# Kernel tuning notes

Hardware: AMD Instinct MI355X
Metric: run time of the kernel (lower is better)

## Reference

```python
import jax, jax.numpy as jnp
import numpy as np

D_MODEL = 1024
D_STATE = 16
D_CONV = 4
EXPAND = 2
D_INNER = EXPAND * D_MODEL
BATCH = 2
SEQ = 4096


def setup_inputs() -> dict:
    key = jax.random.key(0)
    ks = jax.random.split(key, 8)
    def w(k, shape, fan_in):
        return jax.random.normal(k, shape, jnp.float32) * (fan_in ** -0.5)
    x = jax.random.normal(ks[0], (BATCH, SEQ, D_MODEL), jnp.float32)
    in_proj_w = w(ks[1], (2 * D_INNER, D_MODEL), D_MODEL)
    conv_w = w(ks[2], (D_INNER, 1, D_CONV), D_CONV)          # depthwise conv kernel (OIH, groups=D_INNER)
    conv_b = jnp.zeros((D_INNER,), jnp.float32)
    x_proj_w = w(ks[3], (1 + 2 * D_STATE, D_INNER), D_INNER)
    dt_proj_w = w(ks[4], (D_INNER, 1), D_STATE)               # Linear(1 -> d_inner), see notes
    dt_proj_b = jnp.zeros((D_INNER,), jnp.float32)
    A_log = jnp.log(jnp.tile(jnp.arange(1, D_STATE + 1, dtype=jnp.float32)[None, :], (D_INNER, 1)))
    D = jnp.ones((D_INNER,), jnp.float32)
    out_proj_w = w(ks[5], (D_MODEL, D_INNER), D_INNER)
    return dict(x=x, in_proj_w=in_proj_w, conv_w=conv_w, conv_b=conv_b,
                x_proj_w=x_proj_w, dt_proj_w=dt_proj_w, dt_proj_b=dt_proj_b,
                A_log=A_log, D=D, out_proj_w=out_proj_w)


def _selective_scan(xs, delta, Bm, Cm, A, D):
    # xs, delta: [B, L, d_inner]; Bm, Cm: [B, L, d_state]; A: [d_inner, d_state]
    def step(h, inp):
        x_t, d_t, b_t, c_t = inp                      # [B,di],[B,di],[B,n],[B,n]
        dA = jnp.exp(d_t[..., None] * A)              # [B, di, n]
        h = dA * h + (d_t * x_t)[..., None] * b_t[:, None, :]
        y = jnp.einsum('bdn,bn->bd', h, c_t) + D * x_t
        return h, y
    h0 = jnp.zeros((xs.shape[0], xs.shape[2], A.shape[1]), xs.dtype)
    seq = (jnp.swapaxes(xs, 0, 1), jnp.swapaxes(delta, 0, 1),
           jnp.swapaxes(Bm, 0, 1), jnp.swapaxes(Cm, 0, 1))
    _, ys = jax.lax.scan(step, h0, seq)               # ys: [L, B, di]
    return jnp.swapaxes(ys, 0, 1)


def _mamba(x, in_proj_w, conv_w, conv_b, x_proj_w, dt_proj_w, dt_proj_b, A_log, D, out_proj_w):
    xz = x @ in_proj_w.T                               # [B, L, 2*di]
    xc, z = jnp.split(xz, 2, axis=-1)
    # causal depthwise conv (pad left d_conv-1, truncate to seq_len)
    u = jnp.swapaxes(xc, 1, 2)                         # [B, di, L]
    u = jax.lax.conv_general_dilated(
        u, conv_w, window_strides=(1,), padding=[(D_CONV - 1, 0)],
        feature_group_count=D_INNER, dimension_numbers=('NCH', 'OIH', 'NCH'))
    u = u + conv_b[None, :, None]
    xs = jax.nn.silu(jnp.swapaxes(u, 1, 2))            # [B, L, di]
    dbc = xs @ x_proj_w.T                              # [B, L, 1+2n]
    delta_raw = dbc[..., :1]
    Bm = dbc[..., 1:1 + D_STATE]
    Cm = dbc[..., 1 + D_STATE:]
    delta = jax.nn.softplus(delta_raw @ dt_proj_w.T + dt_proj_b)   # [B, L, di]
    A = -jnp.exp(A_log)
    y = _selective_scan(xs, delta, Bm, Cm, A, D)
    return (y * jax.nn.silu(z)) @ out_proj_w.T


def reference(x, in_proj_w, conv_w, conv_b, x_proj_w, dt_proj_w, dt_proj_b, A_log, D, out_proj_w):
    return _mamba(x, in_proj_w, conv_w, conv_b, x_proj_w, dt_proj_w, dt_proj_b, A_log, D, out_proj_w)
```

## Files before the change

kernel.cpp:

```cpp
#include <hip/hip_runtime.h>
#include <hip/hip_bf16.h>
#include <stdint.h>

typedef __bf16 bf16x8 __attribute__((ext_vector_type(8)));
typedef float  f32x4  __attribute__((ext_vector_type(4)));
typedef float  f32x2  __attribute__((ext_vector_type(2)));
typedef unsigned short u16x8 __attribute__((ext_vector_type(8)));

#define TC 32
#define NC 128
#define TH 16

__device__ __forceinline__ unsigned short f2bf(float f) {
  unsigned u = __builtin_bit_cast(unsigned, f);
  unsigned r = (u + 0x7fffu + ((u >> 16) & 1u)) >> 16;
  return (unsigned short)r;
}
__device__ __forceinline__ float bf2f(unsigned short s) {
  unsigned u = ((unsigned)s) << 16;
  return __builtin_bit_cast(float, u);
}

__device__ __forceinline__ void gload_lds16(const void* g, void* l) {
  __builtin_amdgcn_global_load_lds(
      (const __attribute__((address_space(1))) unsigned int*)(g),
      (__attribute__((address_space(3))) unsigned int*)(l),
      16, 0, 0);
}

__global__ __launch_bounds__(256) void prep_k(
    const float4* __restrict__ x, const float4* __restrict__ ipw,
    const float4* __restrict__ opw, const float* __restrict__ xpw,
    ushort4* __restrict__ xb, ushort4* __restrict__ wb1,
    ushort4* __restrict__ wb2, unsigned short* __restrict__ xwp)
{
  const int r = blockIdx.y;
  int i = blockIdx.x * 256 + threadIdx.x;
  const int stride = gridDim.x * 256;
  if (r == 0) {
    for (; i < 2097152; i += stride) {
      float4 v = x[i]; ushort4 o;
      o.x = f2bf(v.x); o.y = f2bf(v.y); o.z = f2bf(v.z); o.w = f2bf(v.w);
      xb[i] = o;
    }
  } else if (r == 1) {
    for (; i < 1048576; i += stride) {
      float4 v = ipw[i]; ushort4 o;
      o.x = f2bf(v.x); o.y = f2bf(v.y); o.z = f2bf(v.z); o.w = f2bf(v.w);
      wb1[i] = o;
    }
  } else if (r == 2) {
    for (; i < 524288; i += stride) {
      float4 v = opw[i]; ushort4 o;
      o.x = f2bf(v.x); o.y = f2bf(v.y); o.z = f2bf(v.z); o.w = f2bf(v.w);
      wb2[i] = o;
    }
  } else {
    for (; i < 262144; i += stride) {
      int row = i >> 11, col = i & 2047;
      xwp[i] = (row < 33) ? f2bf(xpw[row * 2048 + col]) : (unsigned short)0;
    }
  }
}

template <bool BF16OUT, bool SWZ>
__global__ __launch_bounds__(512) void gemm8p(
    const unsigned short* __restrict__ A, const unsigned short* __restrict__ B,
    void* __restrict__ Cv, int M, int N, int K)
{
  __shared__ __align__(16) unsigned short As[2][2][8192];
  __shared__ __align__(16) unsigned short Bs[2][2][8192];
  const int tid = threadIdx.x;

  const int grid_m = M >> 8, grid_n = N >> 8;
  const int nwg = grid_m * grid_n;
  int wid = blockIdx.x;
  if (SWZ) { int q = nwg >> 3; wid = (wid & 7) * q + (wid >> 3); }
  const int GM = 8;
  const int nig = GM * grid_n;
  const int gidg = wid / nig;
  const int rem = wid - gidg * nig;
  const int fm = gidg * GM;
  const int gsz = (grid_m - fm < GM) ? (grid_m - fm) : GM;
  const int pm = fm + rem % gsz;
  const int pn = rem / gsz;
  const int m0 = pm << 8, n0 = pn << 8;

  const int NT = K >> 6;

  const int wq = tid >> 6, l = tid & 63;
  const int wr2 = wq >> 2, wc2 = wq & 3;
  const int lr = l & 15, q16 = l >> 4;
  const int sw = lr & 7;

  const unsigned short* aH0 = A + (size_t)m0 * K;
  const unsigned short* aH1 = A + (size_t)(m0 + 128) * K;
  const unsigned short* bH0 = B + (size_t)n0 * K;
  const unsigned short* bH1 = B + (size_t)(n0 + 128) * K;

#define STAGE8(srcbase, dstp, kt)                                              \
  { _Pragma("unroll") for (int i = 0; i < 2; ++i) {                            \
      int q = tid + 512 * i; int rw = q >> 3; int ssl = (q & 7) ^ (rw & 7);    \
      gload_lds16((srcbase) + (size_t)rw * K + (size_t)(kt) * 64 + ssl * 8,    \
                  (dstp) + q * 8); } }

#define LDA8(dd, MH)                                                           \
  { _Pragma("unroll") for (int mi = 0; mi < 4; ++mi) {                         \
      int ar = (wr2 * 64 + mi * 16 + lr) * 64;                                 \
      _Pragma("unroll") for (int ks = 0; ks < 2; ++ks)                         \
        af[mi][ks] = *(const bf16x8*)&As[dd][MH][ar + (((ks * 4 + q16) ^ sw) << 3)]; } }

#define LDB8(dd, NH)                                                           \
  { _Pragma("unroll") for (int ni = 0; ni < 2; ++ni) {                         \
      int br = (wc2 * 32 + ni * 16 + lr) * 64;                                 \
      _Pragma("unroll") for (int ks = 0; ks < 2; ++ks)                         \
        bf[NH][ni][ks] = *(const bf16x8*)&Bs[dd][NH][br + (((ks * 4 + q16) ^ sw) << 3)]; } }

#define MMA8(MH, NH)                                                           \
  { __builtin_amdgcn_s_setprio(1);                                             \
    _Pragma("unroll") for (int mi = 0; mi < 4; ++mi)                           \
    _Pragma("unroll") for (int ni = 0; ni < 2; ++ni)                           \
    _Pragma("unroll") for (int ks = 0; ks < 2; ++ks)                           \
      acc[MH][NH][mi][ni] = __builtin_amdgcn_mfma_f32_16x16x32_bf16(           \
          af[mi][ks], bf[NH][ni][ks], acc[MH][NH][mi][ni], 0, 0, 0);           \
    __builtin_amdgcn_s_setprio(0); }

  f32x4 acc[2][2][4][2];
#pragma unroll
  for (int a = 0; a < 2; ++a)
#pragma unroll
    for (int b = 0; b < 2; ++b)
#pragma unroll
      for (int c = 0; c < 4; ++c)
#pragma unroll
        for (int d = 0; d < 2; ++d)
          acc[a][b][c][d] = (f32x4){0.f, 0.f, 0.f, 0.f};

  bf16x8 af[4][2];
  bf16x8 bf[2][2][2];

  STAGE8(aH0, As[0][0], 0);
  STAGE8(bH1, Bs[0][1], 0);
  STAGE8(aH1, As[0][1], 0);
  STAGE8(bH0, Bs[0][0], 0);
  if (NT > 1) {
    STAGE8(aH0, As[1][0], 1);
    STAGE8(bH1, Bs[1][1], 1);
    asm volatile("s_waitcnt vmcnt(4)" ::: "memory");
  } else {
    asm volatile("s_waitcnt vmcnt(0)" ::: "memory");
  }
  __builtin_amdgcn_s_barrier();

  for (int t = 0; t < NT; ++t) {
    const int d = t & 1;
    LDA8(d, 0); LDB8(d, 0);
    if (t + 1 < NT) STAGE8(aH1, As[(t + 1) & 1][1], t + 1);
    MMA8(0, 0);
    __builtin_amdgcn_s_barrier();
    LDB8(d, 1);
    if (t + 1 < NT) STAGE8(bH0, Bs[(t + 1) & 1][0], t + 1);
    MMA8(0, 1);
    __builtin_amdgcn_s_barrier();
    LDA8(d, 1);
    if (t + 2 < NT) STAGE8(aH0, As[d][0], t + 2);
    MMA8(1, 1);
    __builtin_amdgcn_s_barrier();
    if (t + 2 < NT) STAGE8(bH1, Bs[d][1], t + 2);
    MMA8(1, 0);
    if (t + 2 < NT) asm volatile("s_waitcnt vmcnt(4)" ::: "memory");
    else            asm volatile("s_waitcnt vmcnt(0)" ::: "memory");
    __builtin_amdgcn_s_barrier();
  }

#pragma unroll
  for (int mh = 0; mh < 2; ++mh)
#pragma unroll
    for (int nh = 0; nh < 2; ++nh)
#pragma unroll
      for (int mi = 0; mi < 4; ++mi)
#pragma unroll
        for (int ni = 0; ni < 2; ++ni) {
          int gr = m0 + mh * 128 + wr2 * 64 + mi * 16 + q16 * 4;
          int gc = n0 + nh * 128 + wc2 * 32 + ni * 16 + lr;
#pragma unroll
          for (int j = 0; j < 4; ++j) {
            if (BF16OUT)
              ((unsigned short*)Cv)[(size_t)(gr + j) * N + gc] = f2bf(acc[mh][nh][mi][ni][j]);
            else
              ((float*)Cv)[(size_t)(gr + j) * N + gc] = acc[mh][nh][mi][ni][j];
          }
        }
#undef STAGE8
#undef LDA8
#undef LDB8
#undef MMA8
}

template <bool BF16OUT, bool SWZ>
__global__ __launch_bounds__(256) void gemm2p(
    const unsigned short* __restrict__ A, const unsigned short* __restrict__ B,
    void* __restrict__ Cv, int M, int N, int K)
{
  __shared__ __align__(16) unsigned short AsB[3 * 128 * 32];
  __shared__ __align__(16) unsigned short BsB[3 * 128 * 32];
  const int tid = threadIdx.x;

  const int grid_m = M >> 7, grid_n = N >> 7;
  const int nwg = grid_m * grid_n;
  int wid = blockIdx.x;
  if (SWZ) { int q = nwg >> 3; wid = (wid & 7) * q + (wid >> 3); }
  const int GM = 16;
  const int nig = GM * grid_n;
  const int gidg = wid / nig;
  const int rem = wid - gidg * nig;
  const int fm = gidg * GM;
  const int gsz = (grid_m - fm < GM) ? (grid_m - fm) : GM;
  const int pm = fm + rem % gsz;
  const int pn = rem / gsz;
  const int m0 = pm << 7, n0 = pn << 7;

  const int kseg = K / gridDim.z;
  const int kbeg = blockIdx.z * kseg;
  const int NT = kseg >> 5;

  const int w = tid >> 6, l = tid & 63;
  const int wr = w >> 1, wc = w & 1;
  const int lr = l & 15, kk = (l >> 4) * 8;

  f32x4 acc[4][4];
#pragma unroll
  for (int mi = 0; mi < 4; ++mi)
#pragma unroll
    for (int ni = 0; ni < 4; ++ni)
      acc[mi][ni] = (f32x4){0.f, 0.f, 0.f, 0.f};

#pragma unroll
  for (int tt = 0; tt < 2; ++tt) {
    unsigned short* as = AsB + tt * 4096;
    unsigned short* bs = BsB + tt * 4096;
    int k0 = kbeg + tt * 32;
#pragma unroll
    for (int i = 0; i < 2; ++i) {
      int q = tid + 256 * i;
      int row = q >> 2, sub = (q & 3) ^ ((q >> 3) & 3);
      gload_lds16(A + (size_t)(m0 + row) * K + k0 + sub * 8, as + q * 8);
      gload_lds16(B + (size_t)(n0 + row) * K + k0 + sub * 8, bs + q * 8);
    }
  }
  asm volatile("s_waitcnt vmcnt(4)\n\ts_barrier" ::: "memory");

  for (int t = 0; t < NT; ++t) {
    if (t + 2 < NT) {
      unsigned short* as = AsB + ((t + 2) % 3) * 4096;
      unsigned short* bs = BsB + ((t + 2) % 3) * 4096;
      int k0 = kbeg + (t + 2) * 32;
#pragma unroll
      for (int i = 0; i < 2; ++i) {
        int q = tid + 256 * i;
        int row = q >> 2, sub = (q & 3) ^ ((q >> 3) & 3);
        gload_lds16(A + (size_t)(m0 + row) * K + k0 + sub * 8, as + q * 8);
        gload_lds16(B + (size_t)(n0 + row) * K + k0 + sub * 8, bs + q * 8);
      }
    }
    const unsigned short* as = AsB + (t % 3) * 4096;
    const unsigned short* bs = BsB + (t % 3) * 4096;
    bf16x8 af[4], bfr[4];
#pragma unroll
    for (int mi = 0; mi < 4; ++mi) {
      int row = wr * 64 + mi * 16 + lr;
      int col = kk ^ (((row >> 1) & 3) << 3);
      af[mi] = *(const bf16x8*)&as[row * 32 + col];
    }
#pragma unroll
    for (int ni = 0; ni < 4; ++ni) {
      int row = wc * 64 + ni * 16 + lr;
      int col = kk ^ (((row >> 1) & 3) << 3);
      bfr[ni] = *(const bf16x8*)&bs[row * 32 + col];
    }
    __builtin_amdgcn_s_setprio(1);
#pragma unroll
    for (int mi = 0; mi < 4; ++mi)
#pragma unroll
      for (int ni = 0; ni < 4; ++ni)
        acc[mi][ni] = __builtin_amdgcn_mfma_f32_16x16x32_bf16(af[mi], bfr[ni], acc[mi][ni], 0, 0, 0);
    __builtin_amdgcn_s_setprio(0);
    if (t + 1 < NT) {
      if (t + 2 < NT) asm volatile("s_waitcnt vmcnt(4)\n\ts_barrier" ::: "memory");
      else            asm volatile("s_waitcnt vmcnt(0)\n\ts_barrier" ::: "memory");
    }
  }

#pragma unroll
  for (int mi = 0; mi < 4; ++mi)
#pragma unroll
    for (int ni = 0; ni < 4; ++ni) {
      int gr = m0 + wr * 64 + mi * 16 + (l >> 4) * 4;
      int gc = n0 + wc * 64 + ni * 16 + (l & 15);
#pragma unroll
      for (int j = 0; j < 4; ++j) {
        if (BF16OUT)
          ((unsigned short*)Cv)[(size_t)(gr + j) * N + gc] = f2bf(acc[mi][ni][j]);
        else
          ((float*)Cv + (size_t)blockIdx.z * M * N)[(size_t)(gr + j) * N + gc] = acc[mi][ni][j];
      }
    }
}

__global__ __launch_bounds__(256) void redux4_k(const float4* __restrict__ part,
                                                float4* __restrict__ out) {
  int i = blockIdx.x * 256 + threadIdx.x;
  const int STR = 262144;
  float4 a = part[i], b = part[i + STR], c = part[i + 2 * STR], d = part[i + 3 * STR];
  out[i] = make_float4(a.x + b.x + c.x + d.x, a.y + b.y + c.y + d.y,
                       a.z + b.z + c.z + d.z, a.w + b.w + c.w + d.w);
}

#define CONV_L 16
__global__ __launch_bounds__(256) void conv_silu_k(
    const unsigned short* __restrict__ xzb, const float* __restrict__ cw,
    const float* __restrict__ cb, unsigned short* __restrict__ xsb)
{
  const int b = blockIdx.y;
  const int l0 = blockIdx.x * CONV_L;
  const int d = threadIdx.x * 8;
  float w[4][8], bias[8];
#pragma unroll
  for (int i = 0; i < 8; ++i) {
    bias[i] = cb[d + i];
#pragma unroll
    for (int j = 0; j < 4; ++j) w[j][i] = cw[(d + i) * 4 + j];
  }
  const size_t rb = (size_t)b * 4096;
  float win[3][8];
#pragma unroll
  for (int j = 0; j < 3; ++j) {
    int l = l0 - 3 + j;
    if (l >= 0) {
      u16x8 v = *(const u16x8*)(xzb + (rb + l) * 4096 + d);
#pragma unroll
      for (int i = 0; i < 8; ++i) win[j][i] = bf2f(v[i]);
    } else {
#pragma unroll
      for (int i = 0; i < 8; ++i) win[j][i] = 0.f;
    }
  }
  for (int l = l0; l < l0 + CONV_L; ++l) {
    u16x8 v = *(const u16x8*)(xzb + (rb + l) * 4096 + d);
    float cur[8]; u16x8 ob;
#pragma unroll
    for (int i = 0; i < 8; ++i) {
      cur[i] = bf2f(v[i]);
      float u = bias[i] + w[0][i] * win[0][i] + w[1][i] * win[1][i]
                        + w[2][i] * win[2][i] + w[3][i] * cur[i];
      float s = u / (1.f + __expf(-u));
      ob[i] = f2bf(s);
    }
    *(u16x8*)(xsb + (rb + l) * 2048 + d) = ob;
#pragma unroll
    for (int i = 0; i < 8; ++i) { win[0][i] = win[1][i]; win[1][i] = win[2][i]; win[2][i] = cur[i]; }
  }
}

__global__ __launch_bounds__(256) void scan_p1(
    const unsigned short* __restrict__ xsb16, const float* __restrict__ dbc,
    const float* __restrict__ dtw, const float* __restrict__ dtb,
    const float* __restrict__ alog,
    float* __restrict__ Sg, float* __restrict__ cdg)
{
  const int chunk = blockIdx.x;
  const int d0 = blockIdx.y * 256;
  const int b = blockIdx.z;
  const int tid = threadIdx.x;
  const size_t rowbase = (size_t)b * 4096 + chunk * TC;

  __shared__ __align__(16) unsigned short xsS[TH][256];
  __shared__ __align__(16) float bS[TC][16];
  __shared__ float drS[TC];

  if (tid < TC) drS[tid] = dbc[(rowbase + tid) * 128];
  for (int i = tid; i < TC * 16; i += 256) {
    int t = i >> 4, q = i & 15;
    bS[t][q] = dbc[(rowbase + t) * 128 + 1 + q];
  }

  const int d = d0 + tid;
  const float wdt = dtw[d], bdt = dtb[d];
  float adn[16];
  bool ok = true;
#pragma unroll
  for (int k = 0; k < 4; ++k) {
    float4 a4 = *(const float4*)(alog + (size_t)d * 16 + k * 4);
    adn[4 * k + 0] = -__expf(a4.x); adn[4 * k + 1] = -__expf(a4.y);
    adn[4 * k + 2] = -__expf(a4.z); adn[4 * k + 3] = -__expf(a4.w);
  }
#pragma unroll
  for (int n = 0; n < 16; ++n)
    ok = ok && (fabsf(adn[n] + (float)(n + 1)) <= 1e-3f * (float)(n + 1));

  f32x2 h2[8];
#pragma unroll
  for (int k = 0; k < 8; ++k) h2[k] = (f32x2){0.f, 0.f};
  float cd = 0.f;

  for (int half = 0; half < 2; ++half) {
    if (half) __syncthreads();
    for (int i = tid; i < TH * 32; i += 256) {
      int tt = i >> 5, q = i & 31;
      *(u16x8*)&xsS[tt][q * 8] =
          *(const u16x8*)(xsb16 + (rowbase + half * TH + tt) * 2048 + d0 + q * 8);
    }
    __syncthreads();

    if (ok) {
      for (int tt = 0; tt < TH; ++tt) {
        int t = half * TH + tt;
        float pre = fmaf(drS[t], wdt, bdt);
        float e = __expf(pre);
        float dlt = (pre > 20.f) ? pre : __logf(1.f + e);
        float xv = bf2f(xsS[tt][tid]);
        float dx = dlt * xv;
        cd += dlt;
        float r = __expf(-dlt);
        float r2 = r * r;
        f32x2 s2 = (f32x2){r2, r2};
        f32x2 rp2[8];
        rp2[0] = (f32x2){r, r2};
#pragma unroll
        for (int k = 1; k < 8; ++k) rp2[k] = rp2[k - 1] * s2;
        f32x4 Bv[4];
#pragma unroll
        for (int k = 0; k < 4; ++k) Bv[k] = ((const f32x4*)&bS[t][0])[k];
        f32x2 dx2 = (f32x2){dx, dx};
#pragma unroll
        for (int k = 0; k < 4; ++k) {
          f32x2 blo = __builtin_shufflevector(Bv[k], Bv[k], 0, 1);
          f32x2 bhi = __builtin_shufflevector(Bv[k], Bv[k], 2, 3);
          h2[2 * k]     = rp2[2 * k]     * h2[2 * k]     + dx2 * blo;
          h2[2 * k + 1] = rp2[2 * k + 1] * h2[2 * k + 1] + dx2 * bhi;
        }
      }
    } else {
      for (int tt = 0; tt < TH; ++tt) {
        int t = half * TH + tt;
        float pre = fmaf(drS[t], wdt, bdt);
        float e = __expf(pre);
        float dlt = (pre > 20.f) ? pre : __logf(1.f + e);
        float xv = bf2f(xsS[tt][tid]);
        float dx = dlt * xv;
        cd += dlt;
        f32x4 Bv[4];
#pragma unroll
        for (int k = 0; k < 4; ++k) Bv[k] = ((const f32x4*)&bS[t][0])[k];
#pragma unroll
        for (int n = 0; n < 16; ++n) {
          float dA = __expf(adn[n] * dlt);
          h2[n >> 1][n & 1] = fmaf(dA, h2[n >> 1][n & 1], dx * Bv[n >> 2][n & 3]);
        }
      }
    }
  }
  cdg[(size_t)(b * NC + chunk) * 2048 + d] = cd;
  float* Sp = Sg + ((size_t)(b * NC + chunk) * 32768 + (size_t)d * 16);
#pragma unroll
  for (int k = 0; k < 4; ++k)
    ((float4*)Sp)[k] = make_float4(h2[2 * k][0], h2[2 * k][1], h2[2 * k + 1][0], h2[2 * k + 1][1]);
}

__global__ __launch_bounds__(256) void scan_p2(
    float* __restrict__ Sg, const float* __restrict__ cdg,
    const float* __restrict__ alog)
{
  int g = blockIdx.x * 256 + threadIdx.x;
  int b = g >> 15, dn = g & 32767;
  int d = dn >> 4;
  float adn = -__expf(alog[dn]);
  float h = 0.f;
  for (int c = 0; c < NC; ++c) {
    size_t o = (size_t)(b * NC + c) * 32768 + dn;
    float S = Sg[o];
    float P = __expf(adn * cdg[(size_t)(b * NC + c) * 2048 + d]);
    Sg[o] = h;
    h = fmaf(P, h, S);
  }
}

__global__ __launch_bounds__(256) void scan_p3(
    const unsigned short* __restrict__ xsb16, const float* __restrict__ dbc,
    const float* __restrict__ dtw, const float* __restrict__ dtb,
    const float* __restrict__ alog, const float* __restrict__ Dp,
    const unsigned short* __restrict__ xzb, const float* __restrict__ Hg,
    unsigned short* __restrict__ gb)
{
  const int chunk = blockIdx.x;
  const int d0 = blockIdx.y * 256;
  const int b = blockIdx.z;
  const int tid = threadIdx.x;
  const size_t rowbase = (size_t)b * 4096 + chunk * TC;

  __shared__ __align__(16) unsigned short xsS[TH][256];
  __shared__ __align__(16) float bcS[TC][32];

  for (int i = tid; i < TC * 32; i += 256) {
    int t = i >> 5, q = i & 31;
    bcS[t][q] = dbc[(rowbase + t) * 128 + 1 + q];
  }

  const int d = d0 + tid;
  const float wdt = dtw[d], bdt = dtb[d], Dd = Dp[d];
  const float* __restrict__ drp = dbc + rowbase * 128;
  float adn[16];
  bool ok = true;
#pragma unroll
  for (int k = 0; k < 4; ++k) {
    float4 a4 = *(const float4*)(alog + (size_t)d * 16 + k * 4);
    adn[4 * k + 0] = -__expf(a4.x); adn[4 * k + 1] = -__expf(a4.y);
    adn[4 * k + 2] = -__expf(a4.z); adn[4 * k + 3] = -__expf(a4.w);
  }
#pragma unroll
  for (int n = 0; n < 16; ++n)
    ok = ok && (fabsf(adn[n] + (float)(n + 1)) <= 1e-3f * (float)(n + 1));

  f32x2 h2[8];
  {
    const float* Hp = Hg + ((size_t)(b * NC + chunk) * 32768 + (size_t)d * 16);
#pragma unroll
    for (int k = 0; k < 4; ++k) {
      float4 h4 = ((const float4*)Hp)[k];
      h2[2 * k]     = (f32x2){h4.x, h4.y};
      h2[2 * k + 1] = (f32x2){h4.z, h4.w};
    }
  }

  for (int half = 0; half < 2; ++half) {
    if (half) __syncthreads();
    for (int i = tid; i < TH * 32; i += 256) {
      int tt = i >> 5, q = i & 31;
      *(u16x8*)&xsS[tt][q * 8] =
          *(const u16x8*)(xsb16 + (rowbase + half * TH + tt) * 2048 + d0 + q * 8);
    }
    __syncthreads();

    if (ok) {
      for (int tt = 0; tt < TH; ++tt) {
        int t = half * TH + tt;
        float pre = fmaf(drp[(size_t)t * 128], wdt, bdt);
        float e = __expf(pre);
        float dlt = (pre > 20.f) ? pre : __logf(1.f + e);
        float xv = bf2f(xsS[tt][tid]);
        float dx = dlt * xv;
        float r = __expf(-dlt);
        float r2 = r * r;
        f32x2 s2 = (f32x2){r2, r2};
        f32x2 rp2[8];
        rp2[0] = (f32x2){r, r2};
#pragma unroll
        for (int k = 1; k < 8; ++k) rp2[k] = rp2[k - 1] * s2;
        f32x4 Bv[4], Cv[4];
#pragma unroll
        for (int k = 0; k < 4; ++k) {
          Bv[k] = ((const f32x4*)&bcS[t][0])[k];
          Cv[k] = ((const f32x4*)&bcS[t][16])[k];
        }
        f32x2 dx2 = (f32x2){dx, dx};
        f32x2 yp2[4];
#pragma unroll
        for (int k = 0; k < 4; ++k) yp2[k] = (f32x2){0.f, 0.f};
#pragma unroll
        for (int k = 0; k < 4; ++k) {
          f32x2 blo = __builtin_shufflevector(Bv[k], Bv[k], 0, 1);
          f32x2 bhi = __builtin_shufflevector(Bv[k], Bv[k], 2, 3);
          f32x2 clo = __builtin_shufflevector(Cv[k], Cv[k], 0, 1);
          f32x2 chi = __builtin_shufflevector(Cv[k], Cv[k], 2, 3);
          h2[2 * k]     = rp2[2 * k]     * h2[2 * k]     + dx2 * blo;
          h2[2 * k + 1] = rp2[2 * k + 1] * h2[2 * k + 1] + dx2 * bhi;
          yp2[k] = h2[2 * k] * clo + yp2[k];
          yp2[k] = h2[2 * k + 1] * chi + yp2[k];
        }
        f32x2 ys = (yp2[0] + yp2[1]) + (yp2[2] + yp2[3]);
        float y = ys[0] + ys[1] + Dd * xv;
        xsS[tt][tid] = f2bf(y);
      }
    } else {
      for (int tt = 0; tt < TH; ++tt) {
        int t = half * TH + tt;
        float pre = fmaf(drp[(size_t)t * 128], wdt, bdt);
        float e = __expf(pre);
        float dlt = (pre > 20.f) ? pre : __logf(1.f + e);
        float xv = bf2f(xsS[tt][tid]);
        float dx = dlt * xv;
        f32x4 Bv[4], Cv[4];
#pragma unroll
        for (int k = 0; k < 4; ++k) {
          Bv[k] = ((const f32x4*)&bcS[t][0])[k];
          Cv[k] = ((const f32x4*)&bcS[t][16])[k];
        }
        float yp[4];
        yp[0] = Dd * xv; yp[1] = 0.f; yp[2] = 0.f; yp[3] = 0.f;
#pragma unroll
        for (int n = 0; n < 16; ++n) {
          float dA = __expf(adn[n] * dlt);
          h2[n >> 1][n & 1] = fmaf(dA, h2[n >> 1][n & 1], dx * Bv[n >> 2][n & 3]);
          yp[n & 3] = fmaf(h2[n >> 1][n & 1], Cv[n >> 2][n & 3], yp[n & 3]);
        }
        float y = (yp[0] + yp[1]) + (yp[2] + yp[3]);
        xsS[tt][tid] = f2bf(y);
      }
    }
    __syncthreads();

    for (int i = tid; i < TH * 32; i += 256) {
      int tt = i >> 5, q = i & 31;
      size_t row = rowbase + half * TH + tt;
      u16x8 yv = *(const u16x8*)&xsS[tt][q * 8];
      u16x8 zv = *(const u16x8*)(xzb + row * 4096 + 2048 + d0 + q * 8);
      u16x8 ov;
#pragma unroll
      for (int j = 0; j < 8; ++j) {
        float z = bf2f(zv[j]);
        float s = z / (1.f + __expf(-z));
        ov[j] = f2bf(bf2f(yv[j]) * s);
      }
      *(u16x8*)(gb + row * 2048 + d0 + q * 8) = ov;
    }
  }
}

extern "C" void kernel_launch(void* const* d_in, const int* in_sizes, int n_in,
                              void* d_out, int out_size, void* d_ws, size_t ws_size,
                              hipStream_t stream) {
  const float* x    = (const float*)d_in[0];
  const float* ipw  = (const float*)d_in[1];
  const float* cw   = (const float*)d_in[2];
  const float* cb   = (const float*)d_in[3];
  const float* xpw  = (const float*)d_in[4];
  const float* dtw  = (const float*)d_in[5];
  const float* dtb  = (const float*)d_in[6];
  const float* alog = (const float*)d_in[7];
  const float* Dp   = (const float*)d_in[8];
  const float* opw  = (const float*)d_in[9];
  float* out = (float*)d_out;

  char* p = (char*)d_ws;
  unsigned short* xb   = (unsigned short*)p; p += (size_t)8388608 * 2;
  unsigned short* wb1  = (unsigned short*)p; p += (size_t)4194304 * 2;
  unsigned short* wb2  = (unsigned short*)p; p += (size_t)2097152 * 2;
  unsigned short* xwp  = (unsigned short*)p; p += (size_t)262144 * 2;
  unsigned short* xzb  = (unsigned short*)p; p += (size_t)33554432 * 2;
  unsigned short* xsb16= (unsigned short*)p; p += (size_t)16777216 * 2;
  float*          dbc  = (float*)p;          p += (size_t)1048576 * 4;
  unsigned short* gb   = (unsigned short*)p; p += (size_t)16777216 * 2;
  float*          Sg   = (float*)p;          p += (size_t)8388608 * 4;
  float*          cdg  = (float*)p;          p += (size_t)524288 * 4;
  float*          dbcp = Sg;

  prep_k<<<dim3(512, 4), 256, 0, stream>>>(
      (const float4*)x, (const float4*)ipw, (const float4*)opw, xpw,
      (ushort4*)xb, (ushort4*)wb1, (ushort4*)wb2, xwp);

  gemm8p<true, true><<<512, 512, 0, stream>>>(xb, wb1, xzb, 8192, 4096, 1024);
  conv_silu_k<<<dim3(4096 / CONV_L, 2), 256, 0, stream>>>(xzb, cw, cb, xsb16);

  gemm2p<false, false><<<dim3(64, 1, 4), 256, 0, stream>>>(xsb16, xwp, dbcp, 8192, 128, 2048);
  redux4_k<<<1024, 256, 0, stream>>>((const float4*)dbcp, (float4*)dbc);

  scan_p1<<<dim3(NC, 8, 2), 256, 0, stream>>>(xsb16, dbc, dtw, dtb, alog, Sg, cdg);
  scan_p2<<<256, 256, 0, stream>>>(Sg, cdg, alog);
  scan_p3<<<dim3(NC, 8, 2), 256, 0, stream>>>(xsb16, dbc, dtw, dtb, alog, Dp, xzb, Sg, gb);

  gemm2p<false, true><<<dim3(512, 1, 1), 256, 0, stream>>>(gb, wb2, out, 8192, 1024, 2048);
}
```

Measured before the change: 282.0 us.

## Simplify GEMM main loop to a single-barrier double-buffered schedule

Replaces the four-phase interleaved schedule of the 256x256 bf16 GEMM kernel with a simpler double-buffered loop. Each iteration loads all A/B fragments for the current tile into registers, issues global-to-LDS staging for the whole next tile, runs all MFMAs, then waits on vmcnt(0) and hits one barrier. This removes three barriers per k-step and the staggered two-tile-ahead prefetch, with the aim of cutting synchronisation overhead. In exchange it holds more fragment registers and gives less overlap between loads and MFMAs, so memory latency may be exposed at the end of each step.

```diff
diff --git a/kernel.cpp b/kernel.cpp
--- a/kernel.cpp
+++ b/kernel.cpp
@@ -104,27 +104,6 @@
       gload_lds16((srcbase) + (size_t)rw * K + (size_t)(kt) * 64 + ssl * 8,    \
                   (dstp) + q * 8); } }
 
-#define LDA8(dd, MH)                                                           \
-  { _Pragma("unroll") for (int mi = 0; mi < 4; ++mi) {                         \
-      int ar = (wr2 * 64 + mi * 16 + lr) * 64;                                 \
-      _Pragma("unroll") for (int ks = 0; ks < 2; ++ks)                         \
-        af[mi][ks] = *(const bf16x8*)&As[dd][MH][ar + (((ks * 4 + q16) ^ sw) << 3)]; } }
-
-#define LDB8(dd, NH)                                                           \
-  { _Pragma("unroll") for (int ni = 0; ni < 2; ++ni) {                         \
-      int br = (wc2 * 32 + ni * 16 + lr) * 64;                                 \
-      _Pragma("unroll") for (int ks = 0; ks < 2; ++ks)                         \
-        bf[NH][ni][ks] = *(const bf16x8*)&Bs[dd][NH][br + (((ks * 4 + q16) ^ sw) << 3)]; } }
-
-#define MMA8(MH, NH)                                                           \
-  { __builtin_amdgcn_s_setprio(1);                                             \
-    _Pragma("unroll") for (int mi = 0; mi < 4; ++mi)                           \
-    _Pragma("unroll") for (int ni = 0; ni < 2; ++ni)                           \
-    _Pragma("unroll") for (int ks = 0; ks < 2; ++ks)                           \
-      acc[MH][NH][mi][ni] = __builtin_amdgcn_mfma_f32_16x16x32_bf16(           \
-          af[mi][ks], bf[NH][ni][ks], acc[MH][NH][mi][ni], 0, 0, 0);           \
-    __builtin_amdgcn_s_setprio(0); }
-
   f32x4 acc[2][2][4][2];
 #pragma unroll
   for (int a = 0; a < 2; ++a)
@@ -136,40 +115,57 @@
         for (int d = 0; d < 2; ++d)
           acc[a][b][c][d] = (f32x4){0.f, 0.f, 0.f, 0.f};
 
-  bf16x8 af[4][2];
-  bf16x8 bf[2][2][2];
+  bf16x8 af2[2][4][2];
+  bf16x8 bf2[2][2][2];
 
   STAGE8(aH0, As[0][0], 0);
-  STAGE8(bH1, Bs[0][1], 0);
   STAGE8(aH1, As[0][1], 0);
   STAGE8(bH0, Bs[0][0], 0);
-  if (NT > 1) {
-    STAGE8(aH0, As[1][0], 1);
-    STAGE8(bH1, Bs[1][1], 1);
-    asm volatile("s_waitcnt vmcnt(4)" ::: "memory");
-  } else {
-    asm volatile("s_waitcnt vmcnt(0)" ::: "memory");
-  }
+  STAGE8(bH1, Bs[0][1], 0);
+  asm volatile("s_waitcnt vmcnt(0)" ::: "memory");
   __builtin_amdgcn_s_barrier();
 
   for (int t = 0; t < NT; ++t) {
     const int d = t & 1;
-    LDA8(d, 0); LDB8(d, 0);
-    if (t + 1 < NT) STAGE8(aH1, As[(t + 1) & 1][1], t + 1);
-    MMA8(0, 0);
-    __builtin_amdgcn_s_barrier();
-    LDB8(d, 1);
-    if (t + 1 < NT) STAGE8(bH0, Bs[(t + 1) & 1][0], t + 1);
-    MMA8(0, 1);
-    __builtin_amdgcn_s_barrier();
-    LDA8(d, 1);
-    if (t + 2 < NT) STAGE8(aH0, As[d][0], t + 2);
-    MMA8(1, 1);
-    __builtin_amdgcn_s_barrier();
-    if (t + 2 < NT) STAGE8(bH1, Bs[d][1], t + 2);
-    MMA8(1, 0);
-    if (t + 2 < NT) asm volatile("s_waitcnt vmcnt(4)" ::: "memory");
-    else            asm volatile("s_waitcnt vmcnt(0)" ::: "memory");
+#pragma unroll
+    for (int MH = 0; MH < 2; ++MH)
+#pragma unroll
+      for (int mi = 0; mi < 4; ++mi) {
+        int ar = (wr2 * 64 + mi * 16 + lr) * 64;
+#pragma unroll
+        for (int ks = 0; ks < 2; ++ks)
+          af2[MH][mi][ks] = *(const bf16x8*)&As[d][MH][ar + (((ks * 4 + q16) ^ sw) << 3)];
+      }
+#pragma unroll
+    for (int NH = 0; NH < 2; ++NH)
+#pragma unroll
+      for (int ni = 0; ni < 2; ++ni) {
+        int br = (wc2 * 32 + ni * 16 + lr) * 64;
+#pragma unroll
+        for (int ks = 0; ks < 2; ++ks)
+          bf2[NH][ni][ks] = *(const bf16x8*)&Bs[d][NH][br + (((ks * 4 + q16) ^ sw) << 3)];
+      }
+    if (t + 1 < NT) {
+      STAGE8(aH0, As[d ^ 1][0], t + 1);
+      STAGE8(aH1, As[d ^ 1][1], t + 1);
+      STAGE8(bH0, Bs[d ^ 1][0], t + 1);
+      STAGE8(bH1, Bs[d ^ 1][1], t + 1);
+    }
+    __builtin_amdgcn_s_setprio(1);
+#pragma unroll
+    for (int MH = 0; MH < 2; ++MH)
+#pragma unroll
+      for (int NH = 0; NH < 2; ++NH)
+#pragma unroll
+        for (int mi = 0; mi < 4; ++mi)
+#pragma unroll
+          for (int ni = 0; ni < 2; ++ni)
+#pragma unroll
+            for (int ks = 0; ks < 2; ++ks)
+              acc[MH][NH][mi][ni] = __builtin_amdgcn_mfma_f32_16x16x32_bf16(
+                  af2[MH][mi][ks], bf2[NH][ni][ks], acc[MH][NH][mi][ni], 0, 0, 0);
+    __builtin_amdgcn_s_setprio(0);
+    asm volatile("s_waitcnt vmcnt(0)" ::: "memory");
     __builtin_amdgcn_s_barrier();
   }
 
@@ -192,9 +188,6 @@
           }
         }
 #undef STAGE8
-#undef LDA8
-#undef LDB8
-#undef MMA8
 }
 
 template <bool BF16OUT, bool SWZ>
```

After: 283.6 us. About the same (+0.6%).

## Simplify GEMM double-buffer pipeline and prefetch loads in chunk-state scan

Applied to the files above, without the earlier changes.

The 256x256 GEMM loop drops its staggered four-phase schedule, which interleaved quarter-tile global-to-LDS stages with intermediate barriers. It now issues all next-tile stages at once after the first LDS reads and waits for everything with a single vmcnt(0) and one barrier per K step. The scan_p2 recurrence gains a software prefetch of the next chunk's state and cumulative-delta values, so the loads overlap the exp/fma chain. The GEMM change cuts barrier count but risks exposing more global load latency, because only one tile is in flight and the loop drains fully every iteration.

```diff
diff --git a/kernel.cpp b/kernel.cpp
--- a/kernel.cpp
+++ b/kernel.cpp
@@ -104,25 +104,25 @@
       gload_lds16((srcbase) + (size_t)rw * K + (size_t)(kt) * 64 + ssl * 8,    \
                   (dstp) + q * 8); } }
 
-#define LDA8(dd, MH)                                                           \
+#define LDA(dd, MH)                                                            \
   { _Pragma("unroll") for (int mi = 0; mi < 4; ++mi) {                         \
       int ar = (wr2 * 64 + mi * 16 + lr) * 64;                                 \
       _Pragma("unroll") for (int ks = 0; ks < 2; ++ks)                         \
         af[mi][ks] = *(const bf16x8*)&As[dd][MH][ar + (((ks * 4 + q16) ^ sw) << 3)]; } }
 
-#define LDB8(dd, NH)                                                           \
+#define LDB(dd, NH)                                                            \
   { _Pragma("unroll") for (int ni = 0; ni < 2; ++ni) {                         \
       int br = (wc2 * 32 + ni * 16 + lr) * 64;                                 \
       _Pragma("unroll") for (int ks = 0; ks < 2; ++ks)                         \
-        bf[NH][ni][ks] = *(const bf16x8*)&Bs[dd][NH][br + (((ks * 4 + q16) ^ sw) << 3)]; } }
-
-#define MMA8(MH, NH)                                                           \
+        bf2[NH][ni][ks] = *(const bf16x8*)&Bs[dd][NH][br + (((ks * 4 + q16) ^ sw) << 3)]; } }
+
+#define MMA(MH, NH)                                                            \
   { __builtin_amdgcn_s_setprio(1);                                             \
     _Pragma("unroll") for (int mi = 0; mi < 4; ++mi)                           \
     _Pragma("unroll") for (int ni = 0; ni < 2; ++ni)                           \
     _Pragma("unroll") for (int ks = 0; ks < 2; ++ks)                           \
       acc[MH][NH][mi][ni] = __builtin_amdgcn_mfma_f32_16x16x32_bf16(           \
-          af[mi][ks], bf[NH][ni][ks], acc[MH][NH][mi][ni], 0, 0, 0);           \
+          af[mi][ks], bf2[NH][ni][ks], acc[MH][NH][mi][ni], 0, 0, 0);          \
     __builtin_amdgcn_s_setprio(0); }
 
   f32x4 acc[2][2][4][2];
@@ -137,39 +137,32 @@
           acc[a][b][c][d] = (f32x4){0.f, 0.f, 0.f, 0.f};
 
   bf16x8 af[4][2];
-  bf16x8 bf[2][2][2];
+  bf16x8 bf2[2][2][2];
 
   STAGE8(aH0, As[0][0], 0);
-  STAGE8(bH1, Bs[0][1], 0);
   STAGE8(aH1, As[0][1], 0);
   STAGE8(bH0, Bs[0][0], 0);
-  if (NT > 1) {
-    STAGE8(aH0, As[1][0], 1);
-    STAGE8(bH1, Bs[1][1], 1);
-    asm volatile("s_waitcnt vmcnt(4)" ::: "memory");
-  } else {
-    asm volatile("s_waitcnt vmcnt(0)" ::: "memory");
-  }
+  STAGE8(bH1, Bs[0][1], 0);
+  asm volatile("s_waitcnt vmcnt(0)" ::: "memory");
   __builtin_amdgcn_s_barrier();
 
   for (int t = 0; t < NT; ++t) {
     const int d = t & 1;
-    LDA8(d, 0); LDB8(d, 0);
-    if (t + 1 < NT) STAGE8(aH1, As[(t + 1) & 1][1], t + 1);
-    MMA8(0, 0);
-    __builtin_amdgcn_s_barrier();
-    LDB8(d, 1);
-    if (t + 1 < NT) STAGE8(bH0, Bs[(t + 1) & 1][0], t + 1);
-    MMA8(0, 1);
-    __builtin_amdgcn_s_barrier();
-    LDA8(d, 1);
-    if (t + 2 < NT) STAGE8(aH0, As[d][0], t + 2);
-    MMA8(1, 1);
-    __builtin_amdgcn_s_barrier();
-    if (t + 2 < NT) STAGE8(bH1, Bs[d][1], t + 2);
-    MMA8(1, 0);
-    if (t + 2 < NT) asm volatile("s_waitcnt vmcnt(4)" ::: "memory");
-    else            asm volatile("s_waitcnt vmcnt(0)" ::: "memory");
+    LDA(d, 0);
+    LDB(d, 0);
+    if (t + 1 < NT) {
+      STAGE8(aH0, As[d ^ 1][0], t + 1);
+      STAGE8(aH1, As[d ^ 1][1], t + 1);
+      STAGE8(bH0, Bs[d ^ 1][0], t + 1);
+      STAGE8(bH1, Bs[d ^ 1][1], t + 1);
+    }
+    MMA(0, 0);
+    LDB(d, 1);
+    MMA(0, 1);
+    LDA(d, 1);
+    MMA(1, 1);
+    MMA(1, 0);
+    asm volatile("s_waitcnt vmcnt(0)" ::: "memory");
     __builtin_amdgcn_s_barrier();
   }
 
@@ -192,9 +185,9 @@
           }
         }
 #undef STAGE8
-#undef LDA8
-#undef LDB8
-#undef MMA8
+#undef LDA
+#undef LDB
+#undef MMA
 }
 
 template <bool BF16OUT, bool SWZ>
@@ -476,12 +469,21 @@
   int d = dn >> 4;
   float adn = -__expf(alog[dn]);
   float h = 0.f;
+  size_t o = (size_t)(b * NC) * 32768 + dn;
+  size_t oc = (size_t)(b * NC) * 2048 + d;
+  float S = Sg[o];
+  float cdv = cdg[oc];
   for (int c = 0; c < NC; ++c) {
-    size_t o = (size_t)(b * NC + c) * 32768 + dn;
-    float S = Sg[o];
-    float P = __expf(adn * cdg[(size_t)(b * NC + c) * 2048 + d]);
+    float Sn = 0.f, cdn = 0.f;
+    if (c + 1 < NC) {
+      Sn = Sg[o + 32768];
+      cdn = cdg[oc + 2048];
+    }
+    float P = __expf(adn * cdv);
     Sg[o] = h;
     h = fmaf(P, h, S);
+    S = Sn; cdv = cdn;
+    o += 32768; oc += 2048;
   }
 }
 
```

Result: slower. 290.3 us (+2.9%).
